# Optimization experiments

Measured on AMD Instinct MI355X. Metric: run time of the kernel, lower is better.

The kernel has to match this reference:

```python
import jax, jax.numpy as jnp
import numpy as np

NUM_HEADS = 12
HEAD_DIM = 64
EPS = 1e-6


def _layernorm(x, g, b):
    mu = jnp.mean(x, axis=-1, keepdims=True)
    var = jnp.mean(jnp.square(x - mu), axis=-1, keepdims=True)
    return (x - mu) * jax.lax.rsqrt(var + EPS) * g + b


def setup_inputs() -> dict:
    key = jax.random.key(0)
    ks = jax.random.split(key, 8)
    D, DFF = 768, 3072
    s = lambda d: 1.0 / np.sqrt(d)
    return {
        "hidden_states": jax.random.normal(ks[0], (4, 2048, D), jnp.float32),
        "ln1_g": jnp.ones((D,), jnp.float32),
        "ln1_b": jnp.zeros((D,), jnp.float32),
        "w_qkv": jax.random.normal(ks[1], (D, 3 * D), jnp.float32) * s(D),
        "b_qkv": jnp.zeros((3 * D,), jnp.float32),
        "w_attn": jax.random.normal(ks[2], (D, D), jnp.float32) * s(D),
        "b_attn": jnp.zeros((D,), jnp.float32),
        "ln2_g": jnp.ones((D,), jnp.float32),
        "ln2_b": jnp.zeros((D,), jnp.float32),
        "w_in": jax.random.normal(ks[3], (D, DFF), jnp.float32) * s(D),
        "b_in": jnp.zeros((DFF,), jnp.float32),
        "w_out": jax.random.normal(ks[4], (DFF, D), jnp.float32) * s(DFF),
        "b_out": jnp.zeros((D,), jnp.float32),
    }


def reference(hidden_states, ln1_g, ln1_b, w_qkv, b_qkv, w_attn, b_attn,
              ln2_g, ln2_b, w_in, b_in, w_out, b_out):
    B, S, D = hidden_states.shape
    residual = hidden_states
    h = _layernorm(hidden_states, ln1_g, ln1_b)
    # QKV: [B,S,3D] -> [B,S,3,H,hd] -> [3,B,H,S,hd]
    qkv = (h @ w_qkv + b_qkv).reshape(B, S, 3, NUM_HEADS, HEAD_DIM)
    qkv = jnp.transpose(qkv, (2, 0, 3, 1, 4))
    scale = HEAD_DIM ** (-0.5)
    q, k, v = qkv[0] * scale, qkv[1], qkv[2]
    scores = jnp.einsum("bhqd,bhkd->bhqk", q, k)
    attn = jax.nn.softmax(scores, axis=-1)
    o = jnp.einsum("bhqk,bhkd->bhqd", attn, v)
    o = jnp.transpose(o, (0, 2, 1, 3)).reshape(B, S, D)
    h = residual + (o @ w_attn + b_attn)
    residual2 = h
    h2 = _layernorm(h, ln2_g, ln2_b)
    h2 = jax.nn.gelu(h2 @ w_in + b_in, approximate=False)
    h2 = h2 @ w_out + b_out
    return residual2 + h2
```

## Files before the change

### kernel.cpp

```cpp
#include <hip/hip_runtime.h>

typedef __bf16 bf16_t;
typedef bf16_t bf16x8 __attribute__((ext_vector_type(8)));
typedef float f32x4 __attribute__((ext_vector_type(4)));
typedef unsigned short ushortx8 __attribute__((ext_vector_type(8)));
typedef unsigned short ushortx4 __attribute__((ext_vector_type(4)));
typedef short short4v __attribute__((ext_vector_type(4)));

union U8 { ushortx4 h[2]; bf16x8 b; ushortx8 u; };
union SV { bf16_t h[4]; short4v s; };

__device__ __forceinline__ unsigned short f2bf(float f) {
  union { bf16_t h; unsigned short u; } cv;
  cv.h = (bf16_t)f;
  return cv.u;
}

__device__ __forceinline__ void gl_lds16(const unsigned short* g, unsigned short* l) {
  __builtin_amdgcn_global_load_lds((const __attribute__((address_space(1))) void*)g,
                                   (__attribute__((address_space(3))) void*)l,
                                   16, 0, 0);
}

__device__ __forceinline__ float gelu_fast(float v) {
  float v3 = v * v * v;
  float z = -2.30211886f * v - 0.102945f * v3;
  float e = exp2f(z);
  return v * __builtin_amdgcn_rcpf(1.0f + e);
}

__global__ __launch_bounds__(256) void ln_kernel(const float* __restrict__ x,
                                                 const float* __restrict__ g,
                                                 const float* __restrict__ b,
                                                 unsigned short* __restrict__ out) {
  int row = blockIdx.x;
  int t = threadIdx.x;
  const float* xr = x + (size_t)row * 768;
  float v0 = xr[t], v1 = xr[t + 256], v2 = xr[t + 512];
  __shared__ float red[4];
  float s = v0 + v1 + v2;
  for (int o = 32; o > 0; o >>= 1) s += __shfl_down(s, o, 64);
  if ((t & 63) == 0) red[t >> 6] = s;
  __syncthreads();
  float mu = (red[0] + red[1] + red[2] + red[3]) * (1.0f / 768.0f);
  __syncthreads();
  float d0 = v0 - mu, d1 = v1 - mu, d2 = v2 - mu;
  s = d0 * d0 + d1 * d1 + d2 * d2;
  for (int o = 32; o > 0; o >>= 1) s += __shfl_down(s, o, 64);
  if ((t & 63) == 0) red[t >> 6] = s;
  __syncthreads();
  float var = (red[0] + red[1] + red[2] + red[3]) * (1.0f / 768.0f);
  float rs = rsqrtf(var + 1e-6f);
  unsigned short* orow = out + (size_t)row * 768;
  orow[t]       = f2bf(d0 * rs * g[t]       + b[t]);
  orow[t + 256] = f2bf(d1 * rs * g[t + 256] + b[t + 256]);
  orow[t + 512] = f2bf(d2 * rs * g[t + 512] + b[t + 512]);
}

__global__ __launch_bounds__(256) void transpose_all(
    const float* __restrict__ w_qkv, const float* __restrict__ w_attn,
    const float* __restrict__ w_in, const float* __restrict__ w_out,
    unsigned short* __restrict__ wqkvT, unsigned short* __restrict__ wattnT,
    unsigned short* __restrict__ winT, unsigned short* __restrict__ woutT) {
  int id = blockIdx.x;
  const float* W; unsigned short* WT; int K, N, nx, ny;
  if (id < 1728)      { W = w_qkv;  WT = wqkvT;  K = 768;  N = 2304; nx = id % 72; ny = id / 72; }
  else if (id < 2304) { id -= 1728; W = w_attn; WT = wattnT; K = 768;  N = 768;  nx = id % 24; ny = id / 24; }
  else if (id < 4608) { id -= 2304; W = w_in;   WT = winT;   K = 768;  N = 3072; nx = id % 96; ny = id / 96; }
  else                { id -= 4608; W = w_out;  WT = woutT;  K = 3072; N = 768;  nx = id % 24; ny = id / 24; }
  __shared__ float tile[32][33];
  int n0 = nx * 32, k0 = ny * 32;
  int tx = threadIdx.x, ty = threadIdx.y;
  for (int i = 0; i < 4; i++)
    tile[ty + i * 8][tx] = W[(size_t)(k0 + ty + i * 8) * N + n0 + tx];
  __syncthreads();
  for (int i = 0; i < 4; i++)
    WT[(size_t)(n0 + ty + i * 8) * K + k0 + tx] = f2bf(tile[tx][ty + i * 8]);
}

template <int EPI, int TM>
__device__ __forceinline__ void gemm_body(const unsigned short* __restrict__ A,
                                          const unsigned short* __restrict__ BT,
                                          const float* __restrict__ bias,
                                          const float* resid,
                                          void* out, unsigned short* vt, int os,
                                          int N, int K) {
  constexpr int MI = TM / 32;
  __shared__ __align__(16) unsigned short smem[TM * 32 + 4096];
  unsigned short* As = smem;
  unsigned short* Bs = smem + TM * 32;

  int t = threadIdx.x;
  int w = t >> 6, lane = t & 63, ln = lane & 15, quad = lane >> 4;
  int wm = w & 1, wn = w >> 1;
  int m0 = blockIdx.y * TM, n0 = blockIdx.x * 128;

  int srow = w * 16 + (lane >> 2);
  int scol = (lane & 3) * 8;
  const unsigned short* gA0 = A + (size_t)(m0 + srow) * K + scol;
  const unsigned short* gA1 = gA0 + (size_t)64 * K;
  const unsigned short* gB0 = BT + (size_t)(n0 + srow) * K + scol;
  const unsigned short* gB1 = gB0 + (size_t)64 * K;
  unsigned short* dA0 = As + w * 512;
  unsigned short* dA1 = As + 2048 + w * 512;
  unsigned short* dB0 = Bs + w * 512;
  unsigned short* dB1 = Bs + 2048 + w * 512;

  f32x4 acc[MI][4];
  f32x4 zero = {0.f, 0.f, 0.f, 0.f};
  for (int mi = 0; mi < MI; mi++)
    for (int ni = 0; ni < 4; ni++) acc[mi][ni] = zero;

  int nk = K >> 5;
  for (int kt = 0; kt < nk; kt++) {
    __syncthreads();
    gl_lds16(gA0, dA0);
    if constexpr (TM == 128) gl_lds16(gA1, dA1);
    gl_lds16(gB0, dB0);
    gl_lds16(gB1, dB1);
    gA0 += 32; gA1 += 32; gB0 += 32; gB1 += 32;
    __syncthreads();
    bf16x8 af[MI], bf[4];
    for (int mi = 0; mi < MI; mi++)
      af[mi] = *(const bf16x8*)&As[(wm * (TM / 2) + mi * 16 + ln) * 32 + quad * 8];
    for (int ni = 0; ni < 4; ni++)
      bf[ni] = *(const bf16x8*)&Bs[(wn * 64 + ni * 16 + ln) * 32 + quad * 8];
    for (int mi = 0; mi < MI; mi++)
      for (int ni = 0; ni < 4; ni++)
        acc[mi][ni] = __builtin_amdgcn_mfma_f32_16x16x32_bf16(af[mi], bf[ni],
                                                              acc[mi][ni], 0, 0, 0);
  }

  if (EPI == 2) {
    float* outp = (float*)out;
    for (int mi = 0; mi < MI; mi++) {
      for (int ni = 0; ni < 4; ni++) {
        int col = n0 + wn * 64 + ni * 16 + ln;
        float bv = bias[col];
        for (int r = 0; r < 4; r++) {
          int row = m0 + wm * (TM / 2) + mi * 16 + quad * 4 + r;
          float v = acc[mi][ni][r] + bv;
          v += resid[(size_t)row * N + col];
          outp[(size_t)row * N + col] = v;
        }
      }
    }
  } else {
    __syncthreads();
    unsigned short* Cs16 = smem + w * 1024;
    unsigned short* outp = (unsigned short*)out;
    for (int mi = 0; mi < MI; mi++) {
      for (int ni = 0; ni < 4; ni++) {
        int col = n0 + wn * 64 + ni * 16 + ln;
        float bv = bias[col];
        for (int r = 0; r < 4; r++) {
          float v = acc[mi][ni][r] + bv;
          if (EPI == 0) {
            if (col < 768) v *= 0.18033688f;
          } else {
            v = gelu_fast(v);
          }
          Cs16[(quad * 4 + r) * 64 + ni * 16 + ln] = f2bf(v);
        }
      }
      __syncthreads();
      if (EPI == 0 && n0 >= 1536) {
        int c = n0 - 1536 + wn * 64 + lane;
        int s0 = m0 + wm * (TM / 2) + mi * 16;
        int bb = s0 >> 11, sl = s0 & 2047;
        ushortx8 lo, hi;
        for (int r = 0; r < 8; r++) lo[r] = Cs16[r * 64 + lane];
        for (int r = 0; r < 8; r++) hi[r] = Cs16[(8 + r) * 64 + lane];
        size_t vbase = ((size_t)(bb * 768 + c)) * 2048 + sl;
        *(ushortx8*)&vt[vbase] = lo;
        *(ushortx8*)&vt[vbase + 8] = hi;
      } else {
        int OS = (EPI == 0) ? os : N;
        for (int j = 0; j < 2; j++) {
          int rrow = j * 8 + (lane >> 3);
          int ch = (lane & 7) * 8;
          ushortx8 pv = *(const ushortx8*)&Cs16[rrow * 64 + ch];
          *(ushortx8*)&outp[(size_t)(m0 + wm * (TM / 2) + mi * 16 + rrow) * OS +
                            n0 + wn * 64 + ch] = pv;
        }
      }
      __syncthreads();
    }
  }
}

__global__ __launch_bounds__(256) void gemm_qkv(const unsigned short* A,
    const unsigned short* BT, const float* bias, void* out, unsigned short* vt,
    int N, int K) {
  gemm_body<0, 128>(A, BT, bias, nullptr, out, vt, 1536, N, K);
}
__global__ __launch_bounds__(256) void gemm_attnout(const unsigned short* A,
    const unsigned short* BT, const float* bias, const float* resid, void* out,
    int N, int K) {
  gemm_body<2, 64>(A, BT, bias, resid, out, nullptr, N, N, K);
}
__global__ __launch_bounds__(256) void gemm_ffn1(const unsigned short* A,
    const unsigned short* BT, const float* bias, void* out, int N, int K) {
  gemm_body<1, 128>(A, BT, bias, nullptr, out, nullptr, N, N, K);
}
__global__ __launch_bounds__(256) void gemm_ffn2(const unsigned short* A,
    const unsigned short* BT, const float* bias, const float* resid, void* out,
    int N, int K) {
  gemm_body<2, 64>(A, BT, bias, resid, out, nullptr, N, N, K);
}

__global__ __launch_bounds__(512, 6) void flash_attn(
    const unsigned short* __restrict__ qk, const unsigned short* __restrict__ v_t,
    unsigned short* __restrict__ o) {
  int qt = blockIdx.x;
  int bh = blockIdx.y;
  int b = bh / 12, h = bh % 12;
  int t = threadIdx.x;
  int w = t >> 6, lane = t & 63, ln = lane & 15, quad = lane >> 4;

  __shared__ __align__(16) unsigned short smem[18432];
  int qw = b * 2048 + qt * 128 + w * 16;

  bf16x8 qf[2];
  for (int kh = 0; kh < 2; kh++)
    qf[kh] = *(const bf16x8*)&qk[(size_t)(qw + ln) * 1536 + h * 64 + kh * 32 + quad * 8];

  f32x4 zero = {0.f, 0.f, 0.f, 0.f};
  f32x4 o_acc[4];
  for (int df = 0; df < 4; df++) o_acc[df] = zero;
  float lrow = 0.0f;

  int sr = t >> 3, sc = (t & 7) * 8;
  for (int kt = 0; kt < 32; kt++) {
    unsigned short* Ks = smem + (kt & 1) * 9216;
    unsigned short* Vt = Ks + 4608;
    int krow0 = b * 2048 + kt * 64;
    ushortx8 kreg = *(const ushortx8*)&qk[(size_t)(krow0 + sr) * 1536 + 768 + h * 64 + sc];
    ushortx8 vreg = *(const ushortx8*)&v_t[(size_t)(bh * 64 + sr) * 2048 + kt * 64 + sc];
    *(ushortx8*)&Ks[sr * 72 + sc] = kreg;
    *(ushortx8*)&Vt[sr * 72 + sc] = vreg;
    __syncthreads();

    f32x4 ST[4];
    for (int kf = 0; kf < 4; kf++) ST[kf] = zero;
    for (int kh = 0; kh < 2; kh++) {
      bf16x8 kA[4];
      for (int kf = 0; kf < 4; kf++)
        kA[kf] = *(const bf16x8*)&Ks[(kf * 16 + ln) * 72 + kh * 32 + quad * 8];
      for (int kf = 0; kf < 4; kf++)
        ST[kf] = __builtin_amdgcn_mfma_f32_16x16x32_bf16(kA[kf], qf[kh], ST[kf], 0, 0, 0);
    }

    short4v pT[4];
    float rs = 0.0f;
    for (int kf = 0; kf < 4; kf++) {
      SV pv;
      for (int r = 0; r < 4; r++) {
        float e = exp2f(ST[kf][r]);
        rs += e;
        pv.h[r] = (bf16_t)e;
      }
      pT[kf] = pv.s;
    }
    rs += __shfl_xor(rs, 16, 64);
    rs += __shfl_xor(rs, 32, 64);
    lrow += rs;

    for (int kf = 0; kf < 4; kf++) {
      short4v vA[4];
      for (int df = 0; df < 4; df++)
        vA[df] = *(const short4v*)&Vt[(df * 16 + ln) * 72 + kf * 16 + quad * 4];
      for (int df = 0; df < 4; df++)
        o_acc[df] = __builtin_amdgcn_mfma_f32_16x16x16bf16_1k(
            vA[df], pT[kf], o_acc[df], 0, 0, 0);
    }
  }

  unsigned short* Osm = smem + w * 1152;
  float inv = 1.0f / lrow;
  for (int df = 0; df < 4; df++)
    for (int r = 0; r < 4; r++)
      Osm[ln * 72 + df * 16 + quad * 4 + r] = f2bf(o_acc[df][r] * inv);
  __syncthreads();
  for (int p = 0; p < 2; p++) {
    int rr = p * 8 + (lane >> 3);
    int ch = (lane & 7) * 8;
    ushortx8 u = *(const ushortx8*)&Osm[rr * 72 + ch];
    *(ushortx8*)&o[(size_t)(qw + rr) * 768 + h * 64 + ch] = u;
  }
}

extern "C" void kernel_launch(void* const* d_in, const int* in_sizes, int n_in,
                              void* d_out, int out_size, void* d_ws, size_t ws_size,
                              hipStream_t stream) {
  const float* hidden = (const float*)d_in[0];
  const float* ln1_g  = (const float*)d_in[1];
  const float* ln1_b  = (const float*)d_in[2];
  const float* w_qkv  = (const float*)d_in[3];
  const float* b_qkv  = (const float*)d_in[4];
  const float* w_attn = (const float*)d_in[5];
  const float* b_attn = (const float*)d_in[6];
  const float* ln2_g  = (const float*)d_in[7];
  const float* ln2_b  = (const float*)d_in[8];
  const float* w_in   = (const float*)d_in[9];
  const float* b_in   = (const float*)d_in[10];
  const float* w_out  = (const float*)d_in[11];
  const float* b_out  = (const float*)d_in[12];
  float* out = (float*)d_out;

  char* ws = (char*)d_ws;
  unsigned short* wqkvT  = (unsigned short*)(ws + 0);
  unsigned short* wattnT = (unsigned short*)(ws + 3538944);
  unsigned short* winT   = (unsigned short*)(ws + 4718592);
  unsigned short* woutT  = (unsigned short*)(ws + 9437184);
  unsigned short* bufX   = (unsigned short*)(ws + 14155776);
  unsigned short* bufBig = (unsigned short*)(ws + 26738688);
  unsigned short* bufQK  = bufBig;
  unsigned short* v_t    = (unsigned short*)(ws + 26738688 + 25165824);

  transpose_all<<<6912, dim3(32, 8), 0, stream>>>(w_qkv, w_attn, w_in, w_out,
                                                  wqkvT, wattnT, winT, woutT);
  ln_kernel<<<8192, 256, 0, stream>>>(hidden, ln1_g, ln1_b, bufX);
  gemm_qkv<<<dim3(18, 64), 256, 0, stream>>>(bufX, wqkvT, b_qkv, (void*)bufQK,
                                             v_t, 2304, 768);
  flash_attn<<<dim3(16, 48), 512, 0, stream>>>(bufQK, v_t, bufX);
  gemm_attnout<<<dim3(6, 128), 256, 0, stream>>>(bufX, wattnT, b_attn, hidden,
                                                 (void*)out, 768, 768);
  ln_kernel<<<8192, 256, 0, stream>>>(out, ln2_g, ln2_b, bufX);
  gemm_ffn1<<<dim3(24, 64), 256, 0, stream>>>(bufX, winT, b_in, (void*)bufBig,
                                              3072, 768);
  gemm_ffn2<<<dim3(6, 128), 256, 0, stream>>>(bufBig, woutT, b_out, out,
                                              (void*)out, 768, 3072);
}
```

Before: 447.8 us.

## Split attention key tiles across warp pairs and prefetch next K/V tile

Restructures the flash attention kernel so each warp handles 32 query rows and half of each 64-key tile. The two halves are reduced through shared memory at the end. The row-sum is now computed with an MFMA against a ones vector instead of shuffles, and the next K/V tile is loaded into registers before the current tile is computed. This reuses each K fragment load across two query fragments and overlaps global loads with compute. In exchange it raises register pressure (launch bound occupancy lowered from 6 to 4) and adds a cross-warp reduction epilogue.

Result: no change. 445.3 us (-0.6%).

```diff
diff --git a/kernel.cpp b/kernel.cpp
--- a/kernel.cpp
+++ b/kernel.cpp
@@ -209,7 +209,7 @@
   gemm_body<2, 64>(A, BT, bias, resid, out, nullptr, N, N, K);
 }
 
-__global__ __launch_bounds__(512, 6) void flash_attn(
+__global__ __launch_bounds__(512, 4) void flash_attn(
     const unsigned short* __restrict__ qk, const unsigned short* __restrict__ v_t,
     unsigned short* __restrict__ o) {
   int qt = blockIdx.x;
@@ -217,76 +217,112 @@
   int b = bh / 12, h = bh % 12;
   int t = threadIdx.x;
   int w = t >> 6, lane = t & 63, ln = lane & 15, quad = lane >> 4;
+  int qg = w & 3, kh2 = w >> 2;
 
   __shared__ __align__(16) unsigned short smem[18432];
-  int qw = b * 2048 + qt * 128 + w * 16;
-
-  bf16x8 qf[2];
-  for (int kh = 0; kh < 2; kh++)
-    qf[kh] = *(const bf16x8*)&qk[(size_t)(qw + ln) * 1536 + h * 64 + kh * 32 + quad * 8];
+  int qrow0 = b * 2048 + qt * 128;
+  int qw = qrow0 + qg * 32;
+
+  bf16x8 qf[2][2];
+  for (int qi = 0; qi < 2; qi++)
+    for (int kh = 0; kh < 2; kh++)
+      qf[qi][kh] = *(const bf16x8*)&qk[(size_t)(qw + qi * 16 + ln) * 1536 +
+                                      h * 64 + kh * 32 + quad * 8];
+
+  SV ones;
+  for (int r = 0; r < 4; r++) ones.h[r] = (bf16_t)1.0f;
 
   f32x4 zero = {0.f, 0.f, 0.f, 0.f};
-  f32x4 o_acc[4];
-  for (int df = 0; df < 4; df++) o_acc[df] = zero;
-  float lrow = 0.0f;
+  f32x4 o_acc[4][2];
+  for (int df = 0; df < 4; df++)
+    for (int qi = 0; qi < 2; qi++) o_acc[df][qi] = zero;
+  f32x4 l_acc[2] = {zero, zero};
 
   int sr = t >> 3, sc = (t & 7) * 8;
+  ushortx8 kreg = *(const ushortx8*)&qk[(size_t)(b * 2048 + sr) * 1536 + 768 + h * 64 + sc];
+  ushortx8 vreg = *(const ushortx8*)&v_t[(size_t)(bh * 64 + sr) * 2048 + sc];
+
   for (int kt = 0; kt < 32; kt++) {
     unsigned short* Ks = smem + (kt & 1) * 9216;
     unsigned short* Vt = Ks + 4608;
-    int krow0 = b * 2048 + kt * 64;
-    ushortx8 kreg = *(const ushortx8*)&qk[(size_t)(krow0 + sr) * 1536 + 768 + h * 64 + sc];
-    ushortx8 vreg = *(const ushortx8*)&v_t[(size_t)(bh * 64 + sr) * 2048 + kt * 64 + sc];
     *(ushortx8*)&Ks[sr * 72 + sc] = kreg;
     *(ushortx8*)&Vt[sr * 72 + sc] = vreg;
     __syncthreads();
-
-    f32x4 ST[4];
-    for (int kf = 0; kf < 4; kf++) ST[kf] = zero;
-    for (int kh = 0; kh < 2; kh++) {
-      bf16x8 kA[4];
-      for (int kf = 0; kf < 4; kf++)
-        kA[kf] = *(const bf16x8*)&Ks[(kf * 16 + ln) * 72 + kh * 32 + quad * 8];
-      for (int kf = 0; kf < 4; kf++)
-        ST[kf] = __builtin_amdgcn_mfma_f32_16x16x32_bf16(kA[kf], qf[kh], ST[kf], 0, 0, 0);
-    }
-
-    short4v pT[4];
-    float rs = 0.0f;
-    for (int kf = 0; kf < 4; kf++) {
-      SV pv;
-      for (int r = 0; r < 4; r++) {
-        float e = exp2f(ST[kf][r]);
-        rs += e;
-        pv.h[r] = (bf16_t)e;
-      }
-      pT[kf] = pv.s;
-    }
-    rs += __shfl_xor(rs, 16, 64);
-    rs += __shfl_xor(rs, 32, 64);
-    lrow += rs;
-
-    for (int kf = 0; kf < 4; kf++) {
-      short4v vA[4];
+    if (kt < 31) {
+      int krow0 = b * 2048 + (kt + 1) * 64;
+      kreg = *(const ushortx8*)&qk[(size_t)(krow0 + sr) * 1536 + 768 + h * 64 + sc];
+      vreg = *(const ushortx8*)&v_t[(size_t)(bh * 64 + sr) * 2048 + (kt + 1) * 64 + sc];
+    }
+
+    for (int kf = 0; kf < 2; kf++) {
+      int krow = kh2 * 32 + kf * 16;
+      f32x4 ST[2] = {zero, zero};
+      for (int kh = 0; kh < 2; kh++) {
+        bf16x8 kA = *(const bf16x8*)&Ks[(krow + ln) * 72 + kh * 32 + quad * 8];
+        for (int qi = 0; qi < 2; qi++)
+          ST[qi] = __builtin_amdgcn_mfma_f32_16x16x32_bf16(kA, qf[qi][kh],
+                                                           ST[qi], 0, 0, 0);
+      }
+      short4v pT[2];
+      for (int qi = 0; qi < 2; qi++) {
+        SV pv;
+        for (int r = 0; r < 4; r++) pv.h[r] = (bf16_t)exp2f(ST[qi][r]);
+        pT[qi] = pv.s;
+        l_acc[qi] = __builtin_amdgcn_mfma_f32_16x16x16bf16_1k(
+            ones.s, pT[qi], l_acc[qi], 0, 0, 0);
+      }
+      for (int df = 0; df < 4; df++) {
+        short4v vA = *(const short4v*)&Vt[(df * 16 + ln) * 72 + krow + quad * 4];
+        for (int qi = 0; qi < 2; qi++)
+          o_acc[df][qi] = __builtin_amdgcn_mfma_f32_16x16x16bf16_1k(
+              vA, pT[qi], o_acc[df][qi], 0, 0, 0);
+      }
+    }
+  }
+
+  __syncthreads();
+  float* fb = (float*)smem;
+  float* fbl = fb + 8192;
+  if (kh2 == 1) {
+    for (int df = 0; df < 4; df++)
+      for (int qi = 0; qi < 2; qi++)
+        for (int r = 0; r < 4; r++)
+          fb[qg * 2048 + (qi * 16 + ln) * 64 + df * 16 + quad * 4 + r] =
+              o_acc[df][qi][r];
+    if (quad == 0)
+      for (int qi = 0; qi < 2; qi++)
+        fbl[qg * 32 + qi * 16 + ln] = l_acc[qi][0];
+  }
+  __syncthreads();
+  float inv[2];
+  if (kh2 == 0) {
+    for (int qi = 0; qi < 2; qi++) {
+      float lt = l_acc[qi][0] + fbl[qg * 32 + qi * 16 + ln];
+      inv[qi] = 1.0f / lt;
+    }
+    for (int df = 0; df < 4; df++)
+      for (int qi = 0; qi < 2; qi++)
+        for (int r = 0; r < 4; r++)
+          o_acc[df][qi][r] += fb[qg * 2048 + (qi * 16 + ln) * 64 + df * 16 + quad * 4 + r];
+  }
+  __syncthreads();
+  if (kh2 == 0) {
+    unsigned short* Osm = smem + qg * 2304;
+    for (int qi = 0; qi < 2; qi++)
       for (int df = 0; df < 4; df++)
-        vA[df] = *(const short4v*)&Vt[(df * 16 + ln) * 72 + kf * 16 + quad * 4];
-      for (int df = 0; df < 4; df++)
-        o_acc[df] = __builtin_amdgcn_mfma_f32_16x16x16bf16_1k(
-            vA[df], pT[kf], o_acc[df], 0, 0, 0);
-    }
-  }
-
-  unsigned short* Osm = smem + w * 1152;
-  float inv = 1.0f / lrow;
-  for (int df = 0; df < 4; df++)
-    for (int r = 0; r < 4; r++)
-      Osm[ln * 72 + df * 16 + quad * 4 + r] = f2bf(o_acc[df][r] * inv);
-  __syncthreads();
-  for (int p = 0; p < 2; p++) {
-    int rr = p * 8 + (lane >> 3);
-    int ch = (lane & 7) * 8;
-    ushortx8 u = *(const ushortx8*)&Osm[rr * 72 + ch];
-    *(ushortx8*)&o[(size_t)(qw + rr) * 768 + h * 64 + ch] = u;
+        for (int r = 0; r < 4; r++)
+          Osm[(qi * 16 + ln) * 72 + df * 16 + quad * 4 + r] =
+              f2bf(o_acc[df][qi][r] * inv[qi]);
+  }
+  __syncthreads();
+  if (kh2 == 0) {
+    unsigned short* Osm = smem + qg * 2304;
+    for (int p2 = 0; p2 < 4; p2++) {
+      int rr = p2 * 8 + (lane >> 3);
+      int ch = (lane & 7) * 8;
+      ushortx8 u = *(const ushortx8*)&Osm[rr * 72 + ch];
+      *(ushortx8*)&o[(size_t)(qw + rr) * 768 + h * 64 + ch] = u;
+    }
   }
 }
 
```
